# Kernel tuning notes

Hardware: AMD Instinct MI355X
Metric: run time of the kernel (lower is better)

The kernel has to match this reference:

```python
import jax, jax.numpy as jnp
import numpy as np

N = 50000   # nodes
E = 800000  # edges
D = 128     # node_channels


def setup_inputs() -> dict:
    key = jax.random.key(0)
    ks = jax.random.split(key, 16)
    s = 1.0 / np.sqrt(D)
    inp = {
        "x": jax.random.normal(ks[0], (N, D), dtype=jnp.float32),
        "edge_index": jax.random.randint(ks[1], (2, E), 0, N, dtype=jnp.int64),
        "eps": jax.random.normal(ks[2], (N, D), dtype=jnp.float32),
    }
    names = ["1", "2", "mu", "logstd", "5", "6"]
    for i, nm in enumerate(names):
        inp[f"W{nm}"] = jax.random.normal(ks[3 + 2 * i], (D, D), dtype=jnp.float32) * s
        inp[f"b{nm}"] = jnp.zeros((D,), dtype=jnp.float32)
    return inp


def _gcn_norm(edge_index, num_nodes):
    # add self-loops, then symmetric normalization deg^{-1/2} (A+I) deg^{-1/2}
    loop = jnp.arange(num_nodes, dtype=edge_index.dtype)
    src = jnp.concatenate([edge_index[0], loop])
    dst = jnp.concatenate([edge_index[1], loop])
    deg = jax.ops.segment_sum(jnp.ones_like(src, dtype=jnp.float32), dst,
                              num_segments=num_nodes)
    dis = jnp.where(deg > 0, jax.lax.rsqrt(deg), 0.0)
    norm = dis[src] * dis[dst]  # [E + N]
    return src, dst, norm


def _gcn(x, W, b, src, dst, norm, num_nodes):
    h = x @ W                              # [N, D] small GEMM
    msg = h[src] * norm[:, None]           # gather + scale, [E+N, D]
    out = jax.ops.segment_sum(msg, dst, num_segments=num_nodes)  # scatter-add
    return out + b


def reference(x, edge_index, eps, W1, b1, W2, b2, Wmu, bmu, Wlogstd, blogstd,
              W5, b5, W6, b6):
    num_nodes = x.shape[0]
    src, dst, norm = _gcn_norm(edge_index, num_nodes)
    g = lambda h, W, b: _gcn(h, W, b, src, dst, norm, num_nodes)

    nodes = jax.nn.relu(g(x, W1, b1))
    nodes = jax.nn.relu(g(nodes, W2, b2))
    mu = g(nodes, Wmu, bmu)
    logstd = g(nodes, Wlogstd, blogstd)
    # reparametrize (training mode), divider = 10
    nodes = mu + eps * jnp.exp(logstd) / 10.0
    nodes = jax.nn.relu(g(nodes, W5, b5))
    nodes = jax.nn.relu(g(nodes, W6, b6))
    return nodes
```

## Files before the change

kernel.cpp:

```cpp
#include <hip/hip_runtime.h>
#include <hip/hip_bf16.h>
#include <cstdint>
#include <cstddef>

#define D 128
#define NWG 200

typedef _Float16 f16;
typedef f16 f16x2 __attribute__((ext_vector_type(2)));
typedef f16 f16x4 __attribute__((ext_vector_type(4)));
typedef f16 f16x8 __attribute__((ext_vector_type(8)));
typedef float f32x4 __attribute__((ext_vector_type(4)));
typedef unsigned short u16;

static inline size_t align256(size_t x){ return (x + 255) & ~(size_t)255; }

__device__ __forceinline__ int detect_is64(const void* ei){
  const int* e32 = (const int*)ei;
  int probe = e32[2 * (threadIdx.x & 31) + 1];
  return (__ballot(probe != 0) == 0ULL) ? 1 : 0;
}

__device__ __forceinline__ void load_edge(const void* ei, int E, int is64, int e, int& s, int& d){
  if (is64) {
    const long long* p = (const long long*)ei;
    s = (int)p[e]; d = (int)p[(size_t)E + e];
  } else {
    const int* p = (const int*)ei;
    s = p[e]; d = p[(size_t)E + e];
  }
}

__global__ __launch_bounds__(256) void passA_hist(
    const void* __restrict__ ei, int E,
    int* __restrict__ glob_hist, int NB,
    const float* __restrict__ Wa, const float* __restrict__ Wb,
    const float* __restrict__ Wc, const float* __restrict__ Wd,
    const float* __restrict__ We, const float* __restrict__ Wf,
    f16* __restrict__ Wt){
  int t = threadIdx.x, wg = blockIdx.x;
  if (wg >= NWG){
    int i = (wg - NWG) * 256 + t;
    int w = i >> 14, rem = i & 16383;
    int n = rem >> 7, k = rem & 127;
    const float* Wp = (w==0)?Wa:(w==1)?Wb:(w==2)?Wc:(w==3)?Wd:(w==4)?We:Wf;
    Wt[i] = (f16)Wp[k*128 + n];
    return;
  }
  __shared__ int cnt[256];
  int is64 = detect_is64(ei);
  cnt[t] = 0;
  __syncthreads();
  int chunk = (E + NWG - 1) / NWG;
  int lo = wg * chunk, hi = min(lo + chunk, E);
  for (int e = lo + t; e < hi; e += 256){
    int s, d;
    load_edge(ei, E, is64, e, s, d);
    atomicAdd(&cnt[d >> 8], 1);
  }
  __syncthreads();
  for (int b = t; b < NB; b += 256)
    glob_hist[b * NWG + wg] = cnt[b];
}

__global__ void scan_partial(const int* __restrict__ src, int* __restrict__ dst,
                             int* __restrict__ blockSums, int L){
  __shared__ int sd[256];
  int t = threadIdx.x;
  int base = blockIdx.x * 1024 + t * 4;
  int v[4]; int s = 0;
  #pragma unroll
  for (int j = 0; j < 4; ++j){ v[j] = (base + j < L) ? src[base + j] : 0; s += v[j]; }
  sd[t] = s; __syncthreads();
  for (int off = 1; off < 256; off <<= 1){
    int x = (t >= off) ? sd[t - off] : 0;
    __syncthreads();
    sd[t] += x;
    __syncthreads();
  }
  int run = sd[t] - s;
  #pragma unroll
  for (int j = 0; j < 4; ++j){
    if (base + j < L) dst[base + j] = run;
    run += v[j];
  }
  if (t == 255) blockSums[blockIdx.x] = sd[255];
}

__global__ void scan_blocksums(int* __restrict__ blockSums, int nblk){
  __shared__ int sd[256];
  int t = threadIdx.x;
  int v = (t < nblk) ? blockSums[t] : 0;
  sd[t] = v; __syncthreads();
  for (int off = 1; off < 256; off <<= 1){
    int x = (t >= off) ? sd[t - off] : 0;
    __syncthreads();
    sd[t] += x;
    __syncthreads();
  }
  if (t < nblk) blockSums[t] = sd[t] - v;
}

__global__ __launch_bounds__(256) void passB_scatter(
    const void* __restrict__ ei, int E,
    const int* __restrict__ bucketOff, const int* __restrict__ blockSums,
    int NB, unsigned* __restrict__ packed){
  __shared__ int cur[256];
  int t = threadIdx.x, wg = blockIdx.x;
  int is64 = detect_is64(ei);
  for (int b = t; b < NB; b += 256){
    int i = b * NWG + wg;
    cur[b] = bucketOff[i] + blockSums[i >> 10];
  }
  __syncthreads();
  int chunk = (E + NWG - 1) / NWG;
  int lo = wg * chunk, hi = min(lo + chunk, E);
  for (int e = lo + t; e < hi; e += 256){
    int s, d;
    load_edge(ei, E, is64, e, s, d);
    int pos = atomicAdd(&cur[d >> 8], 1);
    packed[pos] = (unsigned)s | ((unsigned)(d & 255) << 16);
  }
}

__global__ __launch_bounds__(256) void passC_csr(
    const unsigned* __restrict__ packed, const int* __restrict__ bucketOff,
    const int* __restrict__ blockSums, int NB, int N, int E,
    int* __restrict__ rowptr, float* __restrict__ dis, u16* __restrict__ csr_src,
    const float* __restrict__ x, f16* __restrict__ bufB){
  __shared__ int degl[256];
  __shared__ int sd[256];
  __shared__ int cur[256];
  __shared__ float disl[256];
  int t = threadIdx.x, b = blockIdx.x;
  int i0 = b * NWG, i1 = (b + 1) * NWG;
  int begin = bucketOff[i0] + blockSums[i0 >> 10];
  int endb  = (b == NB - 1) ? E : (bucketOff[i1] + blockSums[i1 >> 10]);
  degl[t] = 0;
  __syncthreads();
  for (int i = begin + t; i < endb; i += 256)
    atomicAdd(&degl[(packed[i] >> 16) & 255], 1);
  __syncthreads();
  int dv = degl[t];
  sd[t] = dv; __syncthreads();
  for (int off = 1; off < 256; off <<= 1){
    int xm = (t >= off) ? sd[t - off] : 0;
    __syncthreads();
    sd[t] += xm;
    __syncthreads();
  }
  int localOff = sd[t] - dv;
  int v = b * 256 + t;
  float dval = rsqrtf((float)(dv + 1));
  disl[t] = dval;
  if (v < N){
    rowptr[v] = begin + localOff;
    dis[v] = dval;
  }
  if (b == NB - 1 && t == 0) rowptr[N] = E;
  cur[t] = begin + localOff;
  __syncthreads();
  for (int i = begin + t; i < endb; i += 256){
    unsigned p = packed[i];
    int pos = atomicAdd(&cur[(p >> 16) & 255], 1);
    csr_src[pos] = (u16)(p & 0xFFFFu);
  }
  for (int i = t; i < 256 * 64; i += 256){
    int vl = i >> 6;
    int c2 = (i & 63) * 2;
    int vv = b * 256 + vl;
    if (vv >= N) break;
    const float* xr = &x[(size_t)vv * D + c2];
    float dvv = disl[vl];
    f16x2 o; o[0] = (f16)(xr[0] * dvv); o[1] = (f16)(xr[1] * dvv);
    *(f16x2*)&bufB[(size_t)vv * D + c2] = o;
  }
}

__global__ __launch_bounds__(256) void agg16(
    const f16* __restrict__ in, f16* __restrict__ out,
    const int* __restrict__ rowptr, const u16* __restrict__ csr_src,
    const float* __restrict__ dis, int N){
  int v = blockIdx.x * 4 + (threadIdx.x >> 6);
  if (v >= N) return;
  int c2 = (threadIdx.x & 63) * 2;
  float dv = dis[v];
  int beg = rowptr[v], end = rowptr[v + 1];
  f16x2 sv = *(const f16x2*)&in[(size_t)v * D + c2];
  float acc0 = (float)sv[0], acc1 = (float)sv[1];
  int e = beg;
  for (; e + 15 < end; e += 16){
    f16x2 h[16];
    #pragma unroll
    for (int j = 0; j < 16; ++j){
      unsigned u = __builtin_nontemporal_load(&csr_src[e + j]);
      h[j] = *(const f16x2*)&in[(size_t)u * D + c2];
    }
    #pragma unroll
    for (int j = 0; j < 16; ++j){ acc0 += (float)h[j][0]; acc1 += (float)h[j][1]; }
  }
  int rem = end - e;
  if (rem > 0){
    int last = end - 1;
    f16x2 h[16];
    #pragma unroll
    for (int j = 0; j < 16; ++j){
      int idx = e + j;
      idx = idx > last ? last : idx;
      unsigned u = __builtin_nontemporal_load(&csr_src[idx]);
      h[j] = *(const f16x2*)&in[(size_t)u * D + c2];
    }
    #pragma unroll
    for (int j = 0; j < 16; ++j){
      acc0 += (j < rem) ? (float)h[j][0] : 0.f;
      acc1 += (j < rem) ? (float)h[j][1] : 0.f;
    }
  }
  f16x2 o; o[0] = (f16)(acc0 * dv); o[1] = (f16)(acc1 * dv);
  __builtin_nontemporal_store(o, (f16x2*)&out[(size_t)v * D + c2]);
}

template<int EPI>
__global__ __launch_bounds__(512) void gemm_mfma(
    const f16* __restrict__ A, const f16* __restrict__ Wt, const float* __restrict__ bias,
    const f16* __restrict__ Wt2, const float* __restrict__ bias2,
    const float* __restrict__ eps, const float* __restrict__ dis,
    f16* __restrict__ out16, float* __restrict__ outf, int N){

  extern __shared__ __align__(16) f16 Ws[];

  int t = threadIdx.x;
  int wave = t >> 6, lane = t & 63;
  int lrow = lane & 15, hi = lane >> 4;
  int pair = wave >> 1, half = wave & 1;
  int r0 = blockIdx.x * 64 + pair * 16;

  f16x8 a[4];
  {
    int rr = min(r0 + lrow, N - 1);
    const f16* arow = &A[(size_t)rr * D + hi * 8];
    #pragma unroll
    for (int s = 0; s < 4; ++s) a[s] = *(const f16x8*)&arow[s * 32];
  }

  {
    int r = t & 127, p = t >> 7;
    const float4* src = (const float4*)&Wt[r * 128 + p * 32];
    f16* dstrow = &Ws[r * 128];
    #pragma unroll
    for (int i = 0; i < 4; ++i){
      int q = p * 4 + i;
      *(float4*)&dstrow[(q ^ (r & 7)) * 8] = src[i];
    }
    if (EPI == 1){
      const float4* src2 = (const float4*)&Wt2[r * 128 + p * 32];
      f16* dstrow2 = &Ws[16384 + r * 128];
      #pragma unroll
      for (int i = 0; i < 4; ++i){
        int q = p * 4 + i;
        *(float4*)&dstrow2[(q ^ (r & 7)) * 8] = src2[i];
      }
    }
  }
  __syncthreads();

  f32x4 c1[4] = {};
  f32x4 c2[4] = {};

  #pragma unroll
  for (int s = 0; s < 4; ++s){
    #pragma unroll
    for (int tti = 0; tti < 4; ++tti){
      int n = (half * 4 + tti) * 16 + lrow;
      int q = (s * 4 + hi) ^ (lrow & 7);
      f16x8 b = *(const f16x8*)&Ws[n * 128 + q * 8];
      c1[tti] = __builtin_amdgcn_mfma_f32_16x16x32_f16(b, a[s], c1[tti], 0, 0, 0);
      if (EPI == 1){
        f16x8 b2 = *(const f16x8*)&Ws[16384 + n * 128 + q * 8];
        c2[tti] = __builtin_amdgcn_mfma_f32_16x16x32_f16(b2, a[s], c2[tti], 0, 0, 0);
      }
    }
  }

  int r = r0 + lrow;
  if (r >= N) return;
  float dv = (EPI == 2) ? 1.f : dis[r];
  int cbase = hi * 4;
  #pragma unroll
  for (int tti = 0; tti < 4; ++tti){
    int n0 = (half * 4 + tti) * 16 + cbase;
    f32x4 bv = *(const f32x4*)&bias[n0];
    if (EPI == 0){
      f16x4 o;
      #pragma unroll
      for (int ii = 0; ii < 4; ++ii)
        o[ii] = (f16)(fmaxf(c1[tti][ii] + bv[ii], 0.f) * dv);
      *(f16x4*)&out16[(size_t)r * D + n0] = o;
    } else if (EPI == 1){
      f32x4 bv2 = *(const f32x4*)&bias2[n0];
      f32x4 e4  = *(const f32x4*)&eps[(size_t)r * D + n0];
      f16x4 o;
      #pragma unroll
      for (int ii = 0; ii < 4; ++ii){
        float mu = c1[tti][ii] + bv[ii];
        float ls = c2[tti][ii] + bv2[ii];
        o[ii] = (f16)((mu + e4[ii] * __expf(ls) * 0.1f) * dv);
      }
      *(f16x4*)&out16[(size_t)r * D + n0] = o;
    } else {
      f32x4 o;
      #pragma unroll
      for (int ii = 0; ii < 4; ++ii)
        o[ii] = fmaxf(c1[tti][ii] + bv[ii], 0.f);
      *(f32x4*)&outf[(size_t)r * D + n0] = o;
    }
  }
}

extern "C" void kernel_launch(void* const* d_in, const int* in_sizes, int n_in,
                              void* d_out, int out_size, void* d_ws, size_t ws_size,
                              hipStream_t stream){
  const float* x   = (const float*)d_in[0];
  const void*  ei  = d_in[1];
  const float* eps = (const float*)d_in[2];
  const float* W1  = (const float*)d_in[3];  const float* b1  = (const float*)d_in[4];
  const float* W2  = (const float*)d_in[5];  const float* b2  = (const float*)d_in[6];
  const float* Wmu = (const float*)d_in[7];  const float* bmu = (const float*)d_in[8];
  const float* Wls = (const float*)d_in[9];  const float* bls = (const float*)d_in[10];
  const float* W5  = (const float*)d_in[11]; const float* b5  = (const float*)d_in[12];
  const float* W6  = (const float*)d_in[13]; const float* b6  = (const float*)d_in[14];

  const int N = in_sizes[0] / D;
  const int E = in_sizes[1] / 2;
  const int NB = (N + 255) >> 8;
  const int L  = NB * NWG;
  float* out = (float*)d_out;

  char* ws = (char*)d_ws;
  size_t off = 0;
  auto alloc = [&](size_t bytes){ char* p = ws + off; off += align256(bytes); return p; };
  int*      glob_hist = (int*)     alloc(((size_t)L + 1) * 4);
  int*      bucketOff = (int*)     alloc(((size_t)L + 1) * 4);
  int*      blockSums = (int*)     alloc(1024);
  int*      rowptr    = (int*)     alloc(((size_t)N + 1) * 4);
  float*    dis       = (float*)   alloc((size_t)N * 4);
  unsigned* packed    = (unsigned*)alloc((size_t)E * 4);
  u16*      csr_src   = (u16*)     alloc((size_t)E * 2);
  f16*      Wt        = (f16*)     alloc((size_t)6 * 128 * 128 * 2);
  f16*      bufA      = (f16*)     alloc((size_t)N * D * 2);
  f16*      bufB      = (f16*)     alloc((size_t)N * D * 2);
  (void)ws_size; (void)n_in; (void)out_size;

  passA_hist<<<NWG + 384, 256, 0, stream>>>(ei, E, glob_hist, NB,
                                            W1, W2, Wmu, Wls, W5, W6, Wt);
  int nblk = (L + 1023) / 1024;
  scan_partial<<<nblk, 256, 0, stream>>>(glob_hist, bucketOff, blockSums, L);
  scan_blocksums<<<1, 256, 0, stream>>>(blockSums, nblk);
  passB_scatter<<<NWG, 256, 0, stream>>>(ei, E, bucketOff, blockSums, NB, packed);
  passC_csr<<<NB, 256, 0, stream>>>(packed, bucketOff, blockSums, NB, N, E,
                                    rowptr, dis, csr_src, x, bufB);

  int aggGrid = (N + 3) / 4;
  int gemmGrid = (N + 63) / 64;
  size_t lds1 = 128 * 128 * sizeof(f16);
  size_t lds2 = 2 * 128 * 128 * sizeof(f16);

  agg16<<<aggGrid, 256, 0, stream>>>(bufB, bufA, rowptr, csr_src, dis, N);
  gemm_mfma<0><<<gemmGrid, 512, lds1, stream>>>(bufA, Wt + 0*16384, b1, nullptr, nullptr, nullptr, dis, bufB, nullptr, N);
  agg16<<<aggGrid, 256, 0, stream>>>(bufB, bufA, rowptr, csr_src, dis, N);
  gemm_mfma<0><<<gemmGrid, 512, lds1, stream>>>(bufA, Wt + 1*16384, b2, nullptr, nullptr, nullptr, dis, bufB, nullptr, N);
  agg16<<<aggGrid, 256, 0, stream>>>(bufB, bufA, rowptr, csr_src, dis, N);
  gemm_mfma<1><<<gemmGrid, 512, lds2, stream>>>(bufA, Wt + 2*16384, bmu, Wt + 3*16384, bls, eps, dis, bufB, nullptr, N);
  agg16<<<aggGrid, 256, 0, stream>>>(bufB, bufA, rowptr, csr_src, dis, N);
  gemm_mfma<0><<<gemmGrid, 512, lds1, stream>>>(bufA, Wt + 4*16384, b5, nullptr, nullptr, nullptr, dis, bufB, nullptr, N);
  agg16<<<aggGrid, 256, 0, stream>>>(bufB, bufA, rowptr, csr_src, dis, N);
  gemm_mfma<2><<<gemmGrid, 512, lds1, stream>>>(bufA, Wt + 5*16384, b6, nullptr, nullptr, nullptr, dis, nullptr, out, N);
}
```

Before: 422.8 us.

## Split aggregation into XCD-aware column slices and move input cast to separate kernel

The aggregation kernel now assigns each block a 32-column slice of the feature dimension, with the slice chosen from blockIdx bits so that blocks landing on the same XCD (round-robin dispatch) touch the same column slice and share L2. Within a wave, four lane groups each handle a quarter of the edges and are combined with cross-lane shuffles. The x-to-f16 scaled cast is moved out of the CSR build kernel into its own vectorized kernel. The cost is four times more blocks, each doing its own row-pointer and index loads, plus one extra launch for the cast.

```diff
diff --git a/kernel.cpp b/kernel.cpp
--- a/kernel.cpp
+++ b/kernel.cpp
@@ -126,12 +126,10 @@
 __global__ __launch_bounds__(256) void passC_csr(
     const unsigned* __restrict__ packed, const int* __restrict__ bucketOff,
     const int* __restrict__ blockSums, int NB, int N, int E,
-    int* __restrict__ rowptr, float* __restrict__ dis, u16* __restrict__ csr_src,
-    const float* __restrict__ x, f16* __restrict__ bufB){
+    int* __restrict__ rowptr, float* __restrict__ dis, u16* __restrict__ csr_src){
   __shared__ int degl[256];
   __shared__ int sd[256];
   __shared__ int cur[256];
-  __shared__ float disl[256];
   int t = threadIdx.x, b = blockIdx.x;
   int i0 = b * NWG, i1 = (b + 1) * NWG;
   int begin = bucketOff[i0] + blockSums[i0 >> 10];
@@ -151,11 +149,9 @@
   }
   int localOff = sd[t] - dv;
   int v = b * 256 + t;
-  float dval = rsqrtf((float)(dv + 1));
-  disl[t] = dval;
   if (v < N){
     rowptr[v] = begin + localOff;
-    dis[v] = dval;
+    dis[v] = rsqrtf((float)(dv + 1));
   }
   if (b == NB - 1 && t == 0) rowptr[N] = E;
   cur[t] = begin + localOff;
@@ -165,59 +161,60 @@
     int pos = atomicAdd(&cur[(p >> 16) & 255], 1);
     csr_src[pos] = (u16)(p & 0xFFFFu);
   }
-  for (int i = t; i < 256 * 64; i += 256){
-    int vl = i >> 6;
-    int c2 = (i & 63) * 2;
-    int vv = b * 256 + vl;
-    if (vv >= N) break;
-    const float* xr = &x[(size_t)vv * D + c2];
-    float dvv = disl[vl];
-    f16x2 o; o[0] = (f16)(xr[0] * dvv); o[1] = (f16)(xr[1] * dvv);
-    *(f16x2*)&bufB[(size_t)vv * D + c2] = o;
-  }
-}
-
-__global__ __launch_bounds__(256) void agg16(
+}
+
+__global__ void cast_scale(const float* __restrict__ in, const float* __restrict__ dis,
+                           f16* __restrict__ out, int n4){
+  int i = blockIdx.x * blockDim.x + threadIdx.x;
+  if (i >= n4) return;
+  float dv = dis[i >> 5];
+  float4 v = ((const float4*)in)[i];
+  f16x4 o; o[0]=(f16)(v.x*dv); o[1]=(f16)(v.y*dv); o[2]=(f16)(v.z*dv); o[3]=(f16)(v.w*dv);
+  ((f16x4*)out)[i] = o;
+}
+
+__global__ __launch_bounds__(256) void agg_xcd(
     const f16* __restrict__ in, f16* __restrict__ out,
     const int* __restrict__ rowptr, const u16* __restrict__ csr_src,
     const float* __restrict__ dis, int N){
-  int v = blockIdx.x * 4 + (threadIdx.x >> 6);
+  int b = blockIdx.x;
+  int x8 = b & 7;
+  int slice = x8 >> 1;
+  int ng = (b >> 3) * 2 + (x8 & 1);
+  int v = ng * 4 + (threadIdx.x >> 6);
   if (v >= N) return;
-  int c2 = (threadIdx.x & 63) * 2;
+  int lane = threadIdx.x & 63;
+  int q  = lane >> 4;
+  int sl = lane & 15;
+  int c0 = slice * 32 + sl * 2;
   float dv = dis[v];
   int beg = rowptr[v], end = rowptr[v + 1];
-  f16x2 sv = *(const f16x2*)&in[(size_t)v * D + c2];
-  float acc0 = (float)sv[0], acc1 = (float)sv[1];
-  int e = beg;
-  for (; e + 15 < end; e += 16){
+  float acc0 = 0.f, acc1 = 0.f;
+  for (int e0 = beg; e0 + q < end; e0 += 64){
     f16x2 h[16];
     #pragma unroll
     for (int j = 0; j < 16; ++j){
-      unsigned u = __builtin_nontemporal_load(&csr_src[e + j]);
-      h[j] = *(const f16x2*)&in[(size_t)u * D + c2];
-    }
-    #pragma unroll
-    for (int j = 0; j < 16; ++j){ acc0 += (float)h[j][0]; acc1 += (float)h[j][1]; }
-  }
-  int rem = end - e;
-  if (rem > 0){
-    int last = end - 1;
-    f16x2 h[16];
+      int idx = e0 + q + 4 * j;
+      int cidx = idx < end ? idx : end - 1;
+      unsigned u = __builtin_nontemporal_load(&csr_src[cidx]);
+      h[j] = *(const f16x2*)&in[(size_t)u * D + c0];
+    }
     #pragma unroll
     for (int j = 0; j < 16; ++j){
-      int idx = e + j;
-      idx = idx > last ? last : idx;
-      unsigned u = __builtin_nontemporal_load(&csr_src[idx]);
-      h[j] = *(const f16x2*)&in[(size_t)u * D + c2];
-    }
-    #pragma unroll
-    for (int j = 0; j < 16; ++j){
-      acc0 += (j < rem) ? (float)h[j][0] : 0.f;
-      acc1 += (j < rem) ? (float)h[j][1] : 0.f;
-    }
-  }
-  f16x2 o; o[0] = (f16)(acc0 * dv); o[1] = (f16)(acc1 * dv);
-  __builtin_nontemporal_store(o, (f16x2*)&out[(size_t)v * D + c2]);
+      bool ok = (e0 + q + 4 * j) < end;
+      acc0 += ok ? (float)h[j][0] : 0.f;
+      acc1 += ok ? (float)h[j][1] : 0.f;
+    }
+  }
+  acc0 += __shfl_xor(acc0, 16); acc1 += __shfl_xor(acc1, 16);
+  acc0 += __shfl_xor(acc0, 32); acc1 += __shfl_xor(acc1, 32);
+  if (q == 0){
+    f16x2 sv = *(const f16x2*)&in[(size_t)v * D + c0];
+    f16x2 o;
+    o[0] = (f16)((acc0 + (float)sv[0]) * dv);
+    o[1] = (f16)((acc1 + (float)sv[1]) * dv);
+    __builtin_nontemporal_store(o, (f16x2*)&out[(size_t)v * D + c0]);
+  }
 }
 
 template<int EPI>
@@ -358,21 +355,24 @@
   scan_blocksums<<<1, 256, 0, stream>>>(blockSums, nblk);
   passB_scatter<<<NWG, 256, 0, stream>>>(ei, E, bucketOff, blockSums, NB, packed);
   passC_csr<<<NB, 256, 0, stream>>>(packed, bucketOff, blockSums, NB, N, E,
-                                    rowptr, dis, csr_src, x, bufB);
-
-  int aggGrid = (N + 3) / 4;
+                                    rowptr, dis, csr_src);
+
+  cast_scale<<<(N * D / 4 + 255) / 256, 256, 0, stream>>>(x, dis, bufB, N * D / 4);
+
+  int ngroups = (N + 3) / 4;
+  int aggGrid = 8 * ((ngroups + 1) / 2);
   int gemmGrid = (N + 63) / 64;
   size_t lds1 = 128 * 128 * sizeof(f16);
   size_t lds2 = 2 * 128 * 128 * sizeof(f16);
 
-  agg16<<<aggGrid, 256, 0, stream>>>(bufB, bufA, rowptr, csr_src, dis, N);
+  agg_xcd<<<aggGrid, 256, 0, stream>>>(bufB, bufA, rowptr, csr_src, dis, N);
   gemm_mfma<0><<<gemmGrid, 512, lds1, stream>>>(bufA, Wt + 0*16384, b1, nullptr, nullptr, nullptr, dis, bufB, nullptr, N);
-  agg16<<<aggGrid, 256, 0, stream>>>(bufB, bufA, rowptr, csr_src, dis, N);
+  agg_xcd<<<aggGrid, 256, 0, stream>>>(bufB, bufA, rowptr, csr_src, dis, N);
   gemm_mfma<0><<<gemmGrid, 512, lds1, stream>>>(bufA, Wt + 1*16384, b2, nullptr, nullptr, nullptr, dis, bufB, nullptr, N);
-  agg16<<<aggGrid, 256, 0, stream>>>(bufB, bufA, rowptr, csr_src, dis, N);
+  agg_xcd<<<aggGrid, 256, 0, stream>>>(bufB, bufA, rowptr, csr_src, dis, N);
   gemm_mfma<1><<<gemmGrid, 512, lds2, stream>>>(bufA, Wt + 2*16384, bmu, Wt + 3*16384, bls, eps, dis, bufB, nullptr, N);
-  agg16<<<aggGrid, 256, 0, stream>>>(bufB, bufA, rowptr, csr_src, dis, N);
+  agg_xcd<<<aggGrid, 256, 0, stream>>>(bufB, bufA, rowptr, csr_src, dis, N);
   gemm_mfma<0><<<gemmGrid, 512, lds1, stream>>>(bufA, Wt + 4*16384, b5, nullptr, nullptr, nullptr, dis, bufB, nullptr, N);
-  agg16<<<aggGrid, 256, 0, stream>>>(bufB, bufA, rowptr, csr_src, dis, N);
+  agg_xcd<<<aggGrid, 256, 0, stream>>>(bufB, bufA, rowptr, csr_src, dis, N);
   gemm_mfma<2><<<gemmGrid, 512, lds1, stream>>>(bufA, Wt + 5*16384, b6, nullptr, nullptr, nullptr, dis, nullptr, out, N);
 }
```

After: 725.5 us. 71.6% more time.
